# Kernel optimization log

Measured on AMD Instinct MI355X. Metric: run time of the kernel, lower is better.

## Reference

```python
import jax, jax.numpy as jnp
import numpy as np

BS, N, GD, ND, ED = 8, 256, 64, 64, 32


def setup_inputs() -> dict:
    key = jax.random.key(0)
    ks = jax.random.split(key, 9)
    p = lambda k, shape: (jax.random.normal(k, shape, dtype=jnp.float32) * 0.05)
    return {
        "u": jax.random.normal(ks[0], (BS, GD), dtype=jnp.float32),
        "V": jax.random.normal(ks[1], (BS, N, ND), dtype=jnp.float32),
        "A": jax.random.normal(ks[2], (BS, N, N, ED), dtype=jnp.float32),
        "W_A": p(ks[3], (ED + 2 * ND + GD, ED)),   # f_A_nn
        "b_A": p(ks[4], (ED,)),
        "W_v": p(ks[5], (ED + ND + GD, ND)),        # f_v_nn
        "b_v": p(ks[6], (ND,)),
        "W_u": p(ks[7], (ED + ND + GD, GD)),        # f_u_nn
        "b_u": p(ks[8], (GD,)),
    }


def reference(u, V, A, W_A, b_A, W_v, b_v, W_u, b_u):
    bs, n, nd = V.shape
    ed = A.shape[-1]
    gd = u.shape[-1]
    # f_A: torch concat order is [A, V_j, V_i, u] where x[b,i,j] uses
    # V_j = V[b,j] (from V.unsqueeze(1).expand) and V_i = V[b,i] (its transpose).
    # Split the linear to avoid materializing the [bs,n,n,224] concat tensor.
    Wa_e = W_A[:ed]
    Wa_vj = W_A[ed:ed + nd]
    Wa_vi = W_A[ed + nd:ed + 2 * nd]
    Wa_u = W_A[ed + 2 * nd:]
    A_prime = jax.nn.relu(
        jnp.einsum("bije,eo->bijo", A, Wa_e)
        + (V @ Wa_vj)[:, None, :, :]   # broadcast over i
        + (V @ Wa_vi)[:, :, None, :]   # broadcast over j
        + (u @ Wa_u)[:, None, None, :]
        + b_A
    )  # [bs, n, n, ed]
    # rho_A_v: mean over dim 1
    A_agg_by_node = A_prime.mean(axis=1)  # [bs, n, ed]
    # f_v
    u_b = jnp.broadcast_to(u[:, None, :], (bs, n, gd))
    xv = jnp.concatenate([A_agg_by_node, V, u_b], axis=-1)
    V_prime = jax.nn.relu(xv @ W_v + b_v)  # [bs, n, nd]
    # rho_A_u, rho_v_u
    A_agg = A_prime.mean(axis=(1, 2))  # [bs, ed]
    v_agg = V_prime.mean(axis=1)       # [bs, nd]
    # f_u
    xu = jnp.concatenate([A_agg, v_agg, u], axis=-1)
    u_prime = jax.nn.relu(xu @ W_u + b_u)  # [bs, gd]
    return (u_prime, V_prime, A_prime)
```

## Files before the change

kernel.cpp:

```cpp
#include <hip/hip_runtime.h>
#include <stdint.h>

#define BS 8
#define NN 256
#define GD 64
#define ND 64
#define ED 32

#define GLOBAL_AS __attribute__((address_space(1)))
#define LDS_AS    __attribute__((address_space(3)))

__global__ __launch_bounds__(256) void k1_proj(
        const float* __restrict__ u, const float* __restrict__ V,
        const float* __restrict__ W_A, const float* __restrict__ b_A,
        float* __restrict__ vj, float* __restrict__ vi, float* __restrict__ up,
        float* __restrict__ colsum) {
    __shared__ float W2[2 * ND][ED];
    __shared__ float Vt[32][ND];
    int t   = threadIdx.x;
    int blk = blockIdx.x;
    int bn0 = blk * 32;
    {
        float4 z4 = make_float4(0.f, 0.f, 0.f, 0.f);
        ((float4*)colsum)[blk * 256 + t] = z4;
        if (blk == 0 && t < 192) ((float4*)(colsum + BS * NN * ED))[t] = z4;
    }
    {
        const float4* src = (const float4*)(W_A + ED * ED);
        float4* dst = (float4*)&W2[0][0];
#pragma unroll
        for (int r = 0; r < 4; ++r) dst[r * 256 + t] = src[r * 256 + t];
    }
    {
        const float4* src = (const float4*)(V + (size_t)bn0 * ND);
        float4* dst = (float4*)&Vt[0][0];
        dst[t]       = src[t];
        dst[256 + t] = src[256 + t];
    }
    __syncthreads();
    int rq  = t >> 6;
    int oo  = t & 63;
    int mat = oo >> 5;
    int o   = oo & 31;
#pragma unroll 2
    for (int p = 0; p < 8; ++p) {
        int rl = p * 4 + rq;
        int bn = bn0 + rl;
        float d0 = 0.f, d1 = 0.f, d2 = 0.f, d3 = 0.f;
#pragma unroll
        for (int k = 0; k < ND; k += 4) {
            d0 = fmaf(Vt[rl][k + 0], W2[mat * ND + k + 0][o], d0);
            d1 = fmaf(Vt[rl][k + 1], W2[mat * ND + k + 1][o], d1);
            d2 = fmaf(Vt[rl][k + 2], W2[mat * ND + k + 2][o], d2);
            d3 = fmaf(Vt[rl][k + 3], W2[mat * ND + k + 3][o], d3);
        }
        float acc = (d0 + d1) + (d2 + d3);
        if (mat == 0) vj[bn * ED + o] = acc;
        else          vi[bn * ED + o] = acc;
    }
    if (blk < 8 && t < 32) {
        float a2 = b_A[t];
#pragma unroll 8
        for (int k = 0; k < GD; ++k)
            a2 = fmaf(u[blk * GD + k], W_A[(ED + 2 * ND + k) * ED + t], a2);
        up[blk * ED + t] = a2;
    }
}

__global__ __launch_bounds__(256) void k2_main(
        const float* __restrict__ A, const float* __restrict__ W_A,
        const float* __restrict__ vj, const float* __restrict__ vi,
        const float* __restrict__ up,
        float* __restrict__ Aprime, float* __restrict__ colsum) {
    __shared__ float tile[16][8][ED];
    __shared__ float vit[16][ED];
    int bid = blockIdx.x;
    int b   = bid >> 9;
    int it  = (bid >> 5) & 15;
    int jc  = bid & 31;
    int t    = threadIdx.x;
    int lane = t & 63;
    int wv   = t >> 6;
    int i0 = it * 16;
    int j0 = jc * 8;

    const float* Asrc = A + ((size_t)(b * NN + i0) * NN + j0) * ED;
#pragma unroll
    for (int r = 0; r < 4; ++r) {
        int il = r * 4 + wv;
        const float* g = Asrc + (size_t)il * NN * ED + lane * 4;
        __builtin_amdgcn_global_load_lds((const GLOBAL_AS void*)g,
                                         (LDS_AS void*)&tile[il][0][0], 16, 0, 0);
    }
    {
        const float* vsrc = vi + (size_t)(b * NN + i0) * ED;
        ((float*)vit)[t]       = vsrc[t];
        ((float*)vit)[t + 256] = vsrc[t + 256];
    }
    int jloc = t >> 5;
    int o    = t & 31;
    int j    = j0 + jloc;
    float w_[ED];
#pragma unroll
    for (int e = 0; e < ED; ++e) w_[e] = W_A[e * ED + o];
    float cj = vj[(b * NN + j) * ED + o] + up[b * ED + o];

    __syncthreads();

    float colacc = 0.f;
    float* Pb = Aprime + ((size_t)(b * NN + i0) * NN + j) * ED + o;
#pragma unroll 2
    for (int ii = 0; ii < 16; ++ii) {
        const float4* lr = (const float4*)(&tile[ii][jloc][0]);
        float d0 = 0.f, d1 = 0.f, d2 = 0.f, d3 = 0.f;
#pragma unroll
        for (int q = 0; q < 8; ++q) {
            float4 f = lr[q];
            d0 = fmaf(f.x, w_[4 * q + 0], d0);
            d1 = fmaf(f.y, w_[4 * q + 1], d1);
            d2 = fmaf(f.z, w_[4 * q + 2], d2);
            d3 = fmaf(f.w, w_[4 * q + 3], d3);
        }
        float v = (d0 + d1) + (d2 + d3) + cj + vit[ii][o];
        v = fmaxf(v, 0.f);
        __builtin_nontemporal_store(v, &Pb[(size_t)ii * NN * ED]);
        colacc += v;
    }
    atomicAdd(&colsum[(b * NN + j) * ED + o], colacc);
}

__global__ __launch_bounds__(256) void k3_vprime(
        const float* __restrict__ V, const float* __restrict__ u,
        const float* __restrict__ W_v, const float* __restrict__ b_v,
        const float* __restrict__ colsum, float* __restrict__ Vprime,
        float* __restrict__ vagg, float* __restrict__ aagg) {
    __shared__ float Wv[ED + ND + GD][ND];
    __shared__ float xv[16][ED + ND + GD + 1];
    __shared__ float vred[4][ND];
    __shared__ float ared[4][ED];
    int t = threadIdx.x;
    {
        const float4* src = (const float4*)W_v;
        float4* dst = (float4*)&Wv[0][0];
#pragma unroll
        for (int r = 0; r < 10; ++r) dst[r * 256 + t] = src[r * 256 + t];
    }
    int bn0 = blockIdx.x * 16;
    int b   = bn0 >> 8;
    int d  = t & 63;
    int rq = t >> 6;
#pragma unroll
    for (int p = 0; p < 4; ++p) {
        int rl = p * 4 + rq;
        int bn = bn0 + rl;
        if (d < 32) xv[rl][d] = colsum[bn * ED + d] * (1.f / 256.f);
        xv[rl][ED + d]      = V[(size_t)bn * ND + d];
        xv[rl][ED + ND + d] = u[b * GD + d];
    }
    __syncthreads();
    float vsum = 0.f;
#pragma unroll 2
    for (int p = 0; p < 4; ++p) {
        int rl = p * 4 + rq;
        float acc = b_v[d];
#pragma unroll 8
        for (int k = 0; k < ED + ND + GD; ++k)
            acc = fmaf(xv[rl][k], Wv[k][d], acc);
        acc = fmaxf(acc, 0.f);
        Vprime[(size_t)(bn0 + rl) * ND + d] = acc;
        vsum += acc;
    }
    vred[rq][d] = vsum;
    if (d < 32) {
        float asum = xv[rq][d] + xv[4 + rq][d] + xv[8 + rq][d] + xv[12 + rq][d];
        ared[rq][d] = asum;
    }
    __syncthreads();
    if (t < 64) {
        atomicAdd(&vagg[b * ND + t],
                  vred[0][t] + vred[1][t] + vred[2][t] + vred[3][t]);
    } else if (t < 96) {
        int o = t - 64;
        atomicAdd(&aagg[b * ED + o],
                  ared[0][o] + ared[1][o] + ared[2][o] + ared[3][o]);
    }
}

__global__ __launch_bounds__(64) void k4_uprime(
        const float* __restrict__ u,
        const float* __restrict__ W_u, const float* __restrict__ b_u,
        const float* __restrict__ vagg, const float* __restrict__ aagg,
        float* __restrict__ uprime) {
    int b = blockIdx.x;
    int t = threadIdx.x;
    __shared__ float xu[ED + ND + GD];
    if (t < 32) xu[t] = aagg[b * ED + t] * (1.f / 256.f);
    xu[ED + t]      = vagg[b * ND + t] * (1.f / 256.f);
    xu[ED + ND + t] = u[b * GD + t];
    __syncthreads();
    float acc = b_u[t];
#pragma unroll 8
    for (int k = 0; k < ED + ND + GD; ++k)
        acc = fmaf(xu[k], W_u[k * GD + t], acc);
    uprime[b * GD + t] = fmaxf(acc, 0.f);
}

extern "C" void kernel_launch(void* const* d_in, const int* in_sizes, int n_in,
                              void* d_out, int out_size, void* d_ws, size_t ws_size,
                              hipStream_t stream) {
    const float* u   = (const float*)d_in[0];
    const float* V   = (const float*)d_in[1];
    const float* A   = (const float*)d_in[2];
    const float* W_A = (const float*)d_in[3];
    const float* b_A = (const float*)d_in[4];
    const float* W_v = (const float*)d_in[5];
    const float* b_v = (const float*)d_in[6];
    const float* W_u = (const float*)d_in[7];
    const float* b_u = (const float*)d_in[8];

    float* out    = (float*)d_out;
    float* uprime = out;
    float* Vprime = out + BS * GD;
    float* Aprime = out + BS * GD + BS * NN * ND;

    float* ws     = (float*)d_ws;
    float* vj     = ws;
    float* vi     = vj + BS * NN * ED;
    float* up     = vi + BS * NN * ED;
    float* colsum = up + BS * ED;
    float* vagg   = colsum + BS * NN * ED;
    float* aagg   = vagg + BS * ND;

    hipLaunchKernelGGL(k1_proj, dim3(64), dim3(256), 0, stream,
                       u, V, W_A, b_A, vj, vi, up, colsum);
    hipLaunchKernelGGL(k2_main, dim3(4096), dim3(256), 0, stream,
                       A, W_A, vj, vi, up, Aprime, colsum);
    hipLaunchKernelGGL(k3_vprime, dim3(128), dim3(256), 0, stream,
                       V, u, W_v, b_v, colsum, Vprime, vagg, aagg);
    hipLaunchKernelGGL(k4_uprime, dim3(BS), dim3(64), 0, stream,
                       u, W_u, b_u, vagg, aagg, uprime);
}
```

Measured before the change: 162.8 us.

## Compute edge projection with bf16 MFMA and direct global loads in k2

Replaces the per-thread FP32 dot products over the edge features with bf16 16x16x32 MFMA instructions. A is loaded straight from global memory into registers and converted to bf16 instead of being staged in LDS. The vj/up and vi bias terms are staged in padded shared arrays, and column sums are reduced with a lane shuffle before the atomics. This reduces ALU work in a kernel dominated by memory traffic, at the cost of bf16 rounding error and narrower store segments.

```diff
diff --git a/kernel.cpp b/kernel.cpp
--- a/kernel.cpp
+++ b/kernel.cpp
@@ -7,8 +7,8 @@
 #define ND 64
 #define ED 32
 
-#define GLOBAL_AS __attribute__((address_space(1)))
-#define LDS_AS    __attribute__((address_space(3)))
+typedef __bf16 bf16x8 __attribute__((ext_vector_type(8)));
+typedef float f32x4 __attribute__((ext_vector_type(4)));
 
 __global__ __launch_bounds__(256) void k1_proj(
         const float* __restrict__ u, const float* __restrict__ V,
@@ -72,8 +72,8 @@
         const float* __restrict__ vj, const float* __restrict__ vi,
         const float* __restrict__ up,
         float* __restrict__ Aprime, float* __restrict__ colsum) {
-    __shared__ float tile[16][8][ED];
-    __shared__ float vit[16][ED];
+    __shared__ float cjt[8][ED + 1];
+    __shared__ float vit[16][ED + 1];
     int bid = blockIdx.x;
     int b   = bid >> 9;
     int it  = (bid >> 5) & 15;
@@ -84,49 +84,76 @@
     int i0 = it * 16;
     int j0 = jc * 8;
 
-    const float* Asrc = A + ((size_t)(b * NN + i0) * NN + j0) * ED;
-#pragma unroll
-    for (int r = 0; r < 4; ++r) {
-        int il = r * 4 + wv;
-        const float* g = Asrc + (size_t)il * NN * ED + lane * 4;
-        __builtin_amdgcn_global_load_lds((const GLOBAL_AS void*)g,
-                                         (LDS_AS void*)&tile[il][0][0], 16, 0, 0);
-    }
-    {
-        const float* vsrc = vi + (size_t)(b * NN + i0) * ED;
-        ((float*)vit)[t]       = vsrc[t];
-        ((float*)vit)[t + 256] = vsrc[t + 256];
-    }
-    int jloc = t >> 5;
-    int o    = t & 31;
-    int j    = j0 + jloc;
-    float w_[ED];
-#pragma unroll
-    for (int e = 0; e < ED; ++e) w_[e] = W_A[e * ED + o];
-    float cj = vj[(b * NN + j) * ED + o] + up[b * ED + o];
-
-    __syncthreads();
-
-    float colacc = 0.f;
-    float* Pb = Aprime + ((size_t)(b * NN + i0) * NN + j) * ED + o;
-#pragma unroll 2
-    for (int ii = 0; ii < 16; ++ii) {
-        const float4* lr = (const float4*)(&tile[ii][jloc][0]);
-        float d0 = 0.f, d1 = 0.f, d2 = 0.f, d3 = 0.f;
-#pragma unroll
-        for (int q = 0; q < 8; ++q) {
-            float4 f = lr[q];
-            d0 = fmaf(f.x, w_[4 * q + 0], d0);
-            d1 = fmaf(f.y, w_[4 * q + 1], d1);
-            d2 = fmaf(f.z, w_[4 * q + 2], d2);
-            d3 = fmaf(f.w, w_[4 * q + 3], d3);
+    {
+        int jl = t >> 5, o = t & 31;
+        cjt[jl][o]     = vj[(b * NN + j0 + jl) * ED + o] + up[b * ED + o];
+        vit[jl][o]     = vi[(b * NN + i0 + jl) * ED + o];
+        vit[jl + 8][o] = vi[(b * NN + i0 + jl + 8) * ED + o];
+    }
+
+    int r    = lane & 15;
+    int kc   = lane >> 4;
+    int o0   = lane & 15;
+    int jl_r = r & 7;
+    int ih_r = r >> 3;
+
+    bf16x8 bf0, bf1;
+#pragma unroll
+    for (int e = 0; e < 8; ++e) {
+        bf0[e] = (__bf16)W_A[(kc * 8 + e) * ED + o0];
+        bf1[e] = (__bf16)W_A[(kc * 8 + e) * ED + 16 + o0];
+    }
+
+    __syncthreads();
+
+    float colA0[4] = {0.f, 0.f, 0.f, 0.f};
+    float colA1[4] = {0.f, 0.f, 0.f, 0.f};
+
+#pragma unroll
+    for (int m = 0; m < 2; ++m) {
+        int mt = wv * 2 + m;
+        int ii = mt * 2 + ih_r;
+        const float* src =
+            A + ((size_t)(b * NN + i0 + ii) * NN + (j0 + jl_r)) * ED + kc * 8;
+        float4 f0 = *(const float4*)src;
+        float4 f1 = *(const float4*)(src + 4);
+        bf16x8 af;
+        af[0] = (__bf16)f0.x; af[1] = (__bf16)f0.y;
+        af[2] = (__bf16)f0.z; af[3] = (__bf16)f0.w;
+        af[4] = (__bf16)f1.x; af[5] = (__bf16)f1.y;
+        af[6] = (__bf16)f1.z; af[7] = (__bf16)f1.w;
+        f32x4 acc0 = {0.f, 0.f, 0.f, 0.f};
+        f32x4 acc1 = {0.f, 0.f, 0.f, 0.f};
+        acc0 = __builtin_amdgcn_mfma_f32_16x16x32_bf16(af, bf0, acc0, 0, 0, 0);
+        acc1 = __builtin_amdgcn_mfma_f32_16x16x32_bf16(af, bf1, acc1, 0, 0, 0);
+#pragma unroll
+        for (int q = 0; q < 4; ++q) {
+            int rr   = (lane >> 4) * 4 + q;
+            int jloc = rr & 7;
+            int iiq  = mt * 2 + (rr >> 3);
+            float* dst =
+                Aprime + ((size_t)(b * NN + i0 + iiq) * NN + (j0 + jloc)) * ED;
+            float v0 = fmaxf(acc0[q] + cjt[jloc][o0] + vit[iiq][o0], 0.f);
+            float v1 = fmaxf(acc1[q] + cjt[jloc][16 + o0] + vit[iiq][16 + o0], 0.f);
+            __builtin_nontemporal_store(v0, dst + o0);
+            __builtin_nontemporal_store(v1, dst + 16 + o0);
+            colA0[q] += v0;
+            colA1[q] += v1;
         }
-        float v = (d0 + d1) + (d2 + d3) + cj + vit[ii][o];
-        v = fmaxf(v, 0.f);
-        __builtin_nontemporal_store(v, &Pb[(size_t)ii * NN * ED]);
-        colacc += v;
-    }
-    atomicAdd(&colsum[(b * NN + j) * ED + o], colacc);
+    }
+#pragma unroll
+    for (int q = 0; q < 4; ++q) {
+        colA0[q] += __shfl_xor(colA0[q], 32, 64);
+        colA1[q] += __shfl_xor(colA1[q], 32, 64);
+    }
+    if (lane < 32) {
+#pragma unroll
+        for (int q = 0; q < 4; ++q) {
+            int jl = (lane >> 4) * 4 + q;
+            atomicAdd(&colsum[(b * NN + j0 + jl) * ED + o0],      colA0[q]);
+            atomicAdd(&colsum[(b * NN + j0 + jl) * ED + 16 + o0], colA1[q]);
+        }
+    }
 }
 
 __global__ __launch_bounds__(256) void k3_vprime(
```

After: 165.8 us. No clear change (+1.9%).
